# Performance work log

Hardware: AMD Instinct MI355X
Metric: run time of the kernel (lower is better)

Reference implementation:

```python
import jax, jax.numpy as jnp
import numpy as np

DIM = 1024
MLP_RATIO = 4
EPS = 1e-6


def rmsnorm(x, w):
    return x * jax.lax.rsqrt(jnp.mean(x * x, axis=-1, keepdims=True) + EPS) * w


def film(x, cond, w, b):
    # cond: [B, D] -> scale/shift: [B, D] each, broadcast over tokens
    ss = cond @ w + b  # [B, 2D]
    scale, shift = jnp.split(ss, 2, axis=-1)
    return x * (1.0 + scale[:, None, :]) + shift[:, None, :]


def setup_inputs() -> dict:
    key = jax.random.key(0)
    ks = jax.random.split(key, 16)
    B, N, D = 4, 2048, DIM
    H = D * MLP_RATIO
    s = lambda fan_in: 1.0 / np.sqrt(fan_in)
    return {
        "x": jax.random.normal(ks[0], (B, N, D), jnp.float32),
        "cond": jax.random.normal(ks[1], (B, D), jnp.float32),
        "norm1_w": jnp.ones((D,), jnp.float32),
        "film1_w": jax.random.normal(ks[2], (D, 2 * D), jnp.float32) * s(D),
        "film1_b": jnp.zeros((2 * D,), jnp.float32),
        "q_w": jax.random.normal(ks[3], (D, D), jnp.float32) * s(D),
        "q_b": jnp.zeros((D,), jnp.float32),
        "k_w": jax.random.normal(ks[4], (D, D), jnp.float32) * s(D),
        "k_b": jnp.zeros((D,), jnp.float32),
        "v_w": jax.random.normal(ks[5], (D, D), jnp.float32) * s(D),
        "v_b": jnp.zeros((D,), jnp.float32),
        "proj_w": jax.random.normal(ks[6], (D, D), jnp.float32) * s(D),
        "proj_b": jnp.zeros((D,), jnp.float32),
        "norm2_w": jnp.ones((D,), jnp.float32),
        "film2_w": jax.random.normal(ks[7], (D, 2 * D), jnp.float32) * s(D),
        "film2_b": jnp.zeros((2 * D,), jnp.float32),
        "mlp_w1": jax.random.normal(ks[8], (D, H), jnp.float32) * s(D),
        "mlp_b1": jnp.zeros((H,), jnp.float32),
        "mlp_w2": jax.random.normal(ks[9], (H, D), jnp.float32) * s(H),
        "mlp_b2": jnp.zeros((D,), jnp.float32),
    }


def reference(x, cond, norm1_w, film1_w, film1_b, q_w, q_b, k_w, k_b, v_w, v_b,
              proj_w, proj_b, norm2_w, film2_w, film2_b, mlp_w1, mlp_b1,
              mlp_w2, mlp_b2):
    B, N, D = x.shape
    x_in = x
    h = film(rmsnorm(x, norm1_w), cond, film1_w, film1_b)
    Q = h @ q_w + q_b
    K = h @ k_w + k_b
    V = h @ v_w + v_b
    scores = jnp.einsum('bnd,bmd->bnm', Q, K) * (D ** -0.5)  # [B,N,N]
    attn = jax.nn.softmax(scores, axis=-1)
    out = jnp.einsum('bnm,bmd->bnd', attn, V)
    x = x_in + (out @ proj_w + proj_b)
    x_in = x
    h = film(rmsnorm(x, norm2_w), cond, film2_w, film2_b)
    h = jax.nn.gelu(h @ mlp_w1 + mlp_b1, approximate=False) @ mlp_w2 + mlp_b2
    return x_in + h
```

## Files before the change

kernel.cpp:

```cpp
#include <hip/hip_runtime.h>
#include <math.h>

typedef unsigned short u16;
typedef __bf16 bf16;
typedef bf16 bf16x8 __attribute__((ext_vector_type(8)));
typedef float f32x4 __attribute__((ext_vector_type(4)));

#define DEV __device__ __forceinline__
#define MFMA(a, b, c) __builtin_amdgcn_mfma_f32_16x16x32_bf16(a, b, c, 0, 0, 0)

DEV u16 f2b(float f) {
  unsigned u = __builtin_bit_cast(unsigned, f);
  u += 0x7fffu + ((u >> 16) & 1u);
  return (u16)(u >> 16);
}
DEV float b2f(u16 h) {
  unsigned u = ((unsigned)h) << 16;
  return __builtin_bit_cast(float, u);
}
DEV float gelu_f(float x) {
  float e = __expf(x * (-1.5957691216f - 0.07135481283f * x * x));
  return x / (1.0f + e);
}

DEV void gl2lds16(const void* g, void* l) {
  __builtin_amdgcn_global_load_lds(
      (const __attribute__((address_space(1))) unsigned int*)g,
      (__attribute__((address_space(3))) unsigned int*)l, 16, 0, 0);
}

struct TDesc { const float* src; u16* dst; int R, C, t0, tx; };
struct T6 { TDesc d[6]; };

__global__ void k_transpose6(T6 td) {
  __shared__ float tile[32][33];
  const int id = blockIdx.x;
  TDesc d = td.d[0];
#pragma unroll
  for (int k = 1; k < 6; ++k)
    if (id >= td.d[k].t0) d = td.d[k];
  const int local = id - d.t0;
  const int c0 = (local % d.tx) * 32, r0 = (local / d.tx) * 32;
  const int tx = threadIdx.x, ty = threadIdx.y;
#pragma unroll
  for (int i = 0; i < 32; i += 8)
    tile[ty + i][tx] = d.src[(long)(r0 + ty + i) * d.C + c0 + tx];
  __syncthreads();
#pragma unroll
  for (int i = 0; i < 32; i += 8)
    d.dst[(long)(c0 + ty + i) * d.R + r0 + tx] = f2b(tile[tx][ty + i]);
}

__global__ __launch_bounds__(256) void k_film_part(const float* __restrict__ cond,
                                                   const float* __restrict__ f1w,
                                                   const float* __restrict__ f2w,
                                                   float* __restrict__ part) {
  const int j = blockIdx.x * 256 + threadIdx.x;
  const int b = blockIdx.y;
  const int z = blockIdx.z;
  const int kz = z & 7;
  const float* fw = (z < 8) ? f1w : f2w;
  const float* cp = cond + b * 1024 + kz * 128;
  const float* wp = fw + (long)kz * 128 * 2048 + j;
  float acc = 0.0f;
#pragma unroll 4
  for (int d = 0; d < 128; ++d) acc = fmaf(cp[d], wp[(long)d * 2048], acc);
  part[((z * 4 + b) << 11) + j] = acc;
}
__global__ __launch_bounds__(256) void k_film_comb(const float* __restrict__ part,
                                                   const float* __restrict__ f1b,
                                                   const float* __restrict__ f2b_,
                                                   float* __restrict__ ss) {
  const int j = blockIdx.x * 256 + threadIdx.x;
  const int b = blockIdx.y & 3, f = blockIdx.y >> 2;
  float a = (f ? f2b_ : f1b)[j];
#pragma unroll
  for (int kz = 0; kz < 8; ++kz) a += part[(((f * 8 + kz) * 4 + b) << 11) + j];
  ss[((f * 4 + b) << 11) + j] = a;
}

template <typename InT>
__global__ __launch_bounds__(256) void k_rmsfilm(const InT* __restrict__ x,
                                                 const float* __restrict__ nw,
                                                 const float* __restrict__ ss,
                                                 u16* __restrict__ h) {
  const int row = blockIdx.x;
  const int b = row >> 11;
  const int t = threadIdx.x;
  float4 v;
  if constexpr (sizeof(InT) == 4) {
    v = ((const float4*)(x + (long)row * 1024))[t];
  } else {
    ushort4 u = ((const ushort4*)(x + (long)row * 1024))[t];
    v = make_float4(b2f(u.x), b2f(u.y), b2f(u.z), b2f(u.w));
  }
  float s = v.x * v.x + v.y * v.y + v.z * v.z + v.w * v.w;
#pragma unroll
  for (int off = 32; off; off >>= 1) s += __shfl_xor(s, off);
  __shared__ float red[4];
  const int wv = t >> 6, lane = t & 63;
  if (lane == 0) red[wv] = s;
  __syncthreads();
  const float tot = red[0] + red[1] + red[2] + red[3];
  const float rn = rsqrtf(tot * (1.0f / 1024.0f) + 1e-6f);
  const float4 w4 = ((const float4*)nw)[t];
  const float4 sc = ((const float4*)(ss + b * 2048))[t];
  const float4 sh = ((const float4*)(ss + b * 2048 + 1024))[t];
  ushort4 o;
  o.x = f2b(v.x * rn * w4.x * (1.0f + sc.x) + sh.x);
  o.y = f2b(v.y * rn * w4.y * (1.0f + sc.y) + sh.y);
  o.z = f2b(v.z * rn * w4.z * (1.0f + sc.z) + sh.z);
  o.w = f2b(v.w * rn * w4.w * (1.0f + sc.w) + sh.w);
  ((ushort4*)(h + (long)row * 1024))[t] = o;
}

__global__ __launch_bounds__(256) void k_softmax(u16* __restrict__ S) {
  u16* p = S + ((long)blockIdx.x << 11);
  const int t = threadIdx.x;
  ushort4 u0 = ((ushort4*)p)[2 * t], u1 = ((ushort4*)p)[2 * t + 1];
  float f[8] = {b2f(u0.x), b2f(u0.y), b2f(u0.z), b2f(u0.w),
                b2f(u1.x), b2f(u1.y), b2f(u1.z), b2f(u1.w)};
  float m = f[0];
#pragma unroll
  for (int i = 1; i < 8; ++i) m = fmaxf(m, f[i]);
#pragma unroll
  for (int off = 32; off; off >>= 1) m = fmaxf(m, __shfl_xor(m, off));
  __shared__ float red[4];
  const int wv = t >> 6, lane = t & 63;
  if (lane == 0) red[wv] = m;
  __syncthreads();
  m = fmaxf(fmaxf(red[0], red[1]), fmaxf(red[2], red[3]));
  float s = 0.0f;
#pragma unroll
  for (int i = 0; i < 8; ++i) {
    f[i] = __expf(f[i] - m);
    s += f[i];
  }
#pragma unroll
  for (int off = 32; off; off >>= 1) s += __shfl_xor(s, off);
  __syncthreads();
  if (lane == 0) red[wv] = s;
  __syncthreads();
  const float inv = 1.0f / (red[0] + red[1] + red[2] + red[3]);
  ushort4 o0, o1;
  o0.x = f2b(f[0] * inv); o0.y = f2b(f[1] * inv);
  o0.z = f2b(f[2] * inv); o0.w = f2b(f[3] * inv);
  o1.x = f2b(f[4] * inv); o1.y = f2b(f[5] * inv);
  o1.z = f2b(f[6] * inv); o1.w = f2b(f[7] * inv);
  ((ushort4*)p)[2 * t] = o0;
  ((ushort4*)p)[2 * t + 1] = o1;
}

enum { EB = 1, ES = 2, EG = 4, ER = 8, EQKV = 16, ERB = 32 };

template <int EPI, typename OutT>
__global__ __launch_bounds__(256, 2) void k_gemm(
    const u16* __restrict__ A, const u16* __restrict__ B, OutT* __restrict__ C,
    const float* __restrict__ bias, const float* __restrict__ bias2,
    const float* __restrict__ bias3, const float* __restrict__ resid,
    u16* __restrict__ Vt, float scale, int N, int K, long sAb, long sBb, long sCb) {
  __shared__ u16 As[128 * 64];
  __shared__ u16 Bs[128 * 64];
  const int tid = threadIdx.x, lane = tid & 63, wv = tid >> 6;
  const int wr = wv >> 1, wc = wv & 1;
  const int r = lane & 15, q = lane >> 4;

  int flat = blockIdx.y * gridDim.x + blockIdx.x;
  const int nxy = gridDim.x * gridDim.y;
  flat = (flat & 7) * (nxy >> 3) + (flat >> 3);
  const int bx = flat % gridDim.x, by = flat / gridDim.x;

  const long bm = (long)by * 128, bn = (long)bx * 128;
  const u16* Ab = A + (long)blockIdx.z * sAb + bm * K;
  const u16* Bb = B + (long)blockIdx.z * sBb + bn * K;

  f32x4 acc[4][4] = {};

  for (int k0 = 0; k0 < K; k0 += 64) {
#pragma unroll
    for (int i = 0; i < 4; ++i) {
      const int c = i * 256 + tid;
      const int row = c >> 3, sp = c & 7;
      const long g = (long)row * K + k0 + ((sp ^ (row & 7)) << 3);
      gl2lds16(Ab + g, As + c * 8);
      gl2lds16(Bb + g, Bs + c * 8);
    }
    __syncthreads();
    bf16x8 a[8], b[8];
#pragma unroll
    for (int kh = 0; kh < 2; ++kh) {
#pragma unroll
      for (int i = 0; i < 4; ++i) {
        const int ar = wr * 64 + i * 16 + r;
        const int br = wc * 64 + i * 16 + r;
        a[kh * 4 + i] = *(const bf16x8*)&As[ar * 64 + ((kh * 4 + q) ^ (ar & 7)) * 8];
        b[kh * 4 + i] = *(const bf16x8*)&Bs[br * 64 + ((kh * 4 + q) ^ (br & 7)) * 8];
      }
    }
#pragma unroll
    for (int kh = 0; kh < 2; ++kh)
#pragma unroll
      for (int mi = 0; mi < 4; ++mi)
#pragma unroll
        for (int ni = 0; ni < 4; ++ni)
          acc[mi][ni] = MFMA(a[kh * 4 + mi], b[kh * 4 + ni], acc[mi][ni]);
    __syncthreads();
  }

  const long cb = (long)blockIdx.z * sCb;
#pragma unroll
  for (int ni = 0; ni < 4; ++ni) {
    const long col = bn + wc * 64 + ni * 16 + r;
    float bv = 0.0f;
    int reg = 0, c = (int)col;
    if constexpr ((EPI & EB) != 0) bv = bias[col];
    if constexpr ((EPI & EQKV) != 0) {
      reg = (int)(col >> 10);
      c = (int)col & 1023;
      bv = (reg == 0) ? bias[c] : (reg == 1) ? bias2[c] : bias3[c];
    }
#pragma unroll
    for (int mi = 0; mi < 4; ++mi) {
#pragma unroll
      for (int j = 0; j < 4; ++j) {
        const long row = bm + wr * 64 + mi * 16 + q * 4 + j;
        float v = acc[mi][ni][j];
        if constexpr ((EPI & ES) != 0) v *= scale;
        if constexpr ((EPI & (EB | EQKV)) != 0) v += bv;
        if constexpr ((EPI & EG) != 0) v = gelu_f(v);
        if constexpr ((EPI & ER) != 0) v += resid[row * N + col];
        if constexpr ((EPI & ERB) != 0) v += b2f(((const u16*)resid)[row * N + col]);
        if constexpr ((EPI & EQKV) != 0) {
          if (reg < 2)
            ((u16*)C)[(long)reg * 8388608 + row * 1024 + c] = f2b(v);
          else
            Vt[((row >> 11) << 21) + ((long)c << 11) + (row & 2047)] = f2b(v);
        } else if constexpr (sizeof(OutT) == 4) {
          C[cb + row * N + col] = v;
        } else {
          C[cb + row * N + col] = f2b(v);
        }
      }
    }
  }
}

extern "C" void kernel_launch(void* const* d_in, const int* in_sizes, int n_in,
                              void* d_out, int out_size, void* d_ws, size_t ws_size,
                              hipStream_t stream) {
  const float* x    = (const float*)d_in[0];
  const float* cond = (const float*)d_in[1];
  const float* n1w  = (const float*)d_in[2];
  const float* f1w  = (const float*)d_in[3];
  const float* f1b  = (const float*)d_in[4];
  const float* qw   = (const float*)d_in[5];
  const float* qb   = (const float*)d_in[6];
  const float* kw   = (const float*)d_in[7];
  const float* kb   = (const float*)d_in[8];
  const float* vw   = (const float*)d_in[9];
  const float* vb   = (const float*)d_in[10];
  const float* pw   = (const float*)d_in[11];
  const float* pb   = (const float*)d_in[12];
  const float* n2w  = (const float*)d_in[13];
  const float* f2w  = (const float*)d_in[14];
  const float* f2b_ = (const float*)d_in[15];
  const float* w1   = (const float*)d_in[16];
  const float* b1   = (const float*)d_in[17];
  const float* w2   = (const float*)d_in[18];
  const float* b2   = (const float*)d_in[19];
  float* out = (float*)d_out;

  char* ws = (char*)d_ws;
  size_t o = 0;
  auto alloc = [&](size_t bytes) {
    size_t ret = o;
    o += (bytes + 255) & ~(size_t)255;
    return ret;
  };
  const long N = 2048, D = 1024, H = 4096;

  u16* qkvT = (u16*)(ws + alloc(3 * D * D * 2));
  u16* pT   = (u16*)(ws + alloc(D * D * 2));
  u16* w1T  = (u16*)(ws + alloc(D * H * 2));
  u16* w2T  = (u16*)(ws + alloc(D * H * 2));
  float* ss   = (float*)(ws + alloc(2 * 4 * 2 * D * 4));
  float* part = (float*)(ws + alloc(16 * 4 * 2 * D * 4));
  u16* h    = (u16*)(ws + alloc(4 * N * D * 2));
  u16* x1b  = (u16*)(ws + alloc(4 * N * D * 2));
  u16* AO   = (u16*)(ws + alloc(4 * N * D * 2));
  const size_t big = o;
  u16* Q    = (u16*)(ws + alloc(4 * N * D * 2));
  u16* Kb   = (u16*)(ws + alloc(4 * N * D * 2));
  u16* Vt   = (u16*)(ws + alloc(4 * N * D * 2));
  u16* S    = (u16*)(ws + alloc(4 * N * N * 2));
  u16* h1   = (u16*)(ws + big);
  (void)ws_size; (void)in_sizes; (void)n_in; (void)out_size; (void)Kb;

  T6 td;
  td.d[0] = {qw, qkvT,                1024, 1024,    0,  32};
  td.d[1] = {kw, qkvT + 1024 * 1024,  1024, 1024, 1024,  32};
  td.d[2] = {vw, qkvT + 2048 * 1024,  1024, 1024, 2048,  32};
  td.d[3] = {pw, pT,                  1024, 1024, 3072,  32};
  td.d[4] = {w1, w1T,                 1024, 4096, 4096, 128};
  td.d[5] = {w2, w2T,                 4096, 1024, 8192,  32};
  k_transpose6<<<12288, dim3(32, 8), 0, stream>>>(td);

  k_film_part<<<dim3(8, 4, 16), 256, 0, stream>>>(cond, f1w, f2w, part);
  k_film_comb<<<dim3(8, 8), 256, 0, stream>>>(part, f1b, f2b_, ss);

  k_rmsfilm<float><<<8192, 256, 0, stream>>>(x, n1w, ss, h);

  k_gemm<EQKV, u16><<<dim3(24, 64, 1), 256, 0, stream>>>(
      h, qkvT, Q, qb, kb, vb, nullptr, Vt, 1.0f, 3072, 1024, 0, 0, 0);

  k_gemm<ES, u16><<<dim3(16, 16, 4), 256, 0, stream>>>(
      Q, Kb, S, nullptr, nullptr, nullptr, nullptr, nullptr, 0.03125f,
      2048, 1024, N * D, N * D, N * N);
  k_softmax<<<8192, 256, 0, stream>>>(S);

  k_gemm<0, u16><<<dim3(8, 16, 4), 256, 0, stream>>>(
      S, Vt, AO, nullptr, nullptr, nullptr, nullptr, nullptr, 1.0f,
      1024, 2048, N * N, D * N, N * D);

  k_gemm<EB | ER, u16><<<dim3(8, 64, 1), 256, 0, stream>>>(
      AO, pT, x1b, pb, nullptr, nullptr, x, nullptr, 1.0f, 1024, 1024, 0, 0, 0);

  k_rmsfilm<u16><<<8192, 256, 0, stream>>>(x1b, n2w, ss + 4 * 2048, h);

  k_gemm<EB | EG, u16><<<dim3(32, 64, 1), 256, 0, stream>>>(
      h, w1T, h1, b1, nullptr, nullptr, nullptr, nullptr, 1.0f, 4096, 1024, 0, 0, 0);

  k_gemm<EB | ERB, float><<<dim3(8, 64, 1), 256, 0, stream>>>(
      h1, w2T, out, b2, nullptr, nullptr, (const float*)x1b, nullptr, 1.0f, 1024, 4096, 0, 0, 0);
}
```

Measured before the change: 394.7 us.

## Split PV GEMM over K halves and fold the reduction into projection GEMM

The attention PV GEMM is split along its 2048-long key dimension into two 1024-wide halves. Each half writes its own partial output, which doubles the grid to 16x16x4 blocks. The projection GEMM then runs with K=2048 against a duplicated projection weight, so it sums the two partials itself. This targets low occupancy and a short grid in the PV GEMM. The cost is extra work and traffic in the projection GEMM, and the partials are rounded to bf16 before they are summed. Launch bounds also change from 2 to 4 blocks per CU, which may cause register pressure or spills.

Result: slower. 411.9 us (+4.4%).

```diff
diff --git a/kernel.cpp b/kernel.cpp
--- a/kernel.cpp
+++ b/kernel.cpp
@@ -29,7 +29,7 @@
       (__attribute__((address_space(3))) unsigned int*)l, 16, 0, 0);
 }
 
-struct TDesc { const float* src; u16* dst; int R, C, t0, tx; };
+struct TDesc { const float* src; u16* dst; int R, C, t0, tx, dstLd, dup; };
 struct T6 { TDesc d[6]; };
 
 __global__ void k_transpose6(T6 td) {
@@ -47,8 +47,12 @@
     tile[ty + i][tx] = d.src[(long)(r0 + ty + i) * d.C + c0 + tx];
   __syncthreads();
 #pragma unroll
-  for (int i = 0; i < 32; i += 8)
-    d.dst[(long)(c0 + ty + i) * d.R + r0 + tx] = f2b(tile[tx][ty + i]);
+  for (int i = 0; i < 32; i += 8) {
+    const u16 v = f2b(tile[tx][ty + i]);
+    u16* p = d.dst + (long)(c0 + ty + i) * d.dstLd + r0 + tx;
+    p[0] = v;
+    if (d.dup) p[d.R] = v;
+  }
 }
 
 __global__ __launch_bounds__(256) void k_film_part(const float* __restrict__ cond,
@@ -151,10 +155,10 @@
   ((ushort4*)p)[2 * t + 1] = o1;
 }
 
-enum { EB = 1, ES = 2, EG = 4, ER = 8, EQKV = 16, ERB = 32 };
+enum { EB = 1, ES = 2, EG = 4, ER = 8, EQKV = 16, ERB = 32, EPV = 64 };
 
 template <int EPI, typename OutT>
-__global__ __launch_bounds__(256, 2) void k_gemm(
+__global__ __launch_bounds__(256, 4) void k_gemm(
     const u16* __restrict__ A, const u16* __restrict__ B, OutT* __restrict__ C,
     const float* __restrict__ bias, const float* __restrict__ bias2,
     const float* __restrict__ bias3, const float* __restrict__ resid,
@@ -171,8 +175,11 @@
   const int bx = flat % gridDim.x, by = flat / gridDim.x;
 
   const long bm = (long)by * 128, bn = (long)bx * 128;
-  const u16* Ab = A + (long)blockIdx.z * sAb + bm * K;
-  const u16* Bb = B + (long)blockIdx.z * sBb + bn * K;
+  const long lda = (EPI & EPV) ? 2048 : K;
+  const long kof = (EPI & EPV) ? ((bn >> 10) << 10) : 0;
+  const long bnB = (EPI & EPV) ? (bn & 1023) : bn;
+  const u16* Ab = A + (long)blockIdx.z * sAb + bm * lda;
+  const u16* Bb = B + (long)blockIdx.z * sBb + bnB * lda;
 
   f32x4 acc[4][4] = {};
 
@@ -181,7 +188,7 @@
     for (int i = 0; i < 4; ++i) {
       const int c = i * 256 + tid;
       const int row = c >> 3, sp = c & 7;
-      const long g = (long)row * K + k0 + ((sp ^ (row & 7)) << 3);
+      const long g = (long)row * lda + kof + k0 + ((sp ^ (row & 7)) << 3);
       gl2lds16(Ab + g, As + c * 8);
       gl2lds16(Bb + g, Bs + c * 8);
     }
@@ -280,29 +287,29 @@
   const long N = 2048, D = 1024, H = 4096;
 
   u16* qkvT = (u16*)(ws + alloc(3 * D * D * 2));
-  u16* pT   = (u16*)(ws + alloc(D * D * 2));
+  u16* pT2  = (u16*)(ws + alloc(D * 2 * D * 2));
   u16* w1T  = (u16*)(ws + alloc(D * H * 2));
   u16* w2T  = (u16*)(ws + alloc(D * H * 2));
   float* ss   = (float*)(ws + alloc(2 * 4 * 2 * D * 4));
   float* part = (float*)(ws + alloc(16 * 4 * 2 * D * 4));
   u16* h    = (u16*)(ws + alloc(4 * N * D * 2));
   u16* x1b  = (u16*)(ws + alloc(4 * N * D * 2));
-  u16* AO   = (u16*)(ws + alloc(4 * N * D * 2));
   const size_t big = o;
   u16* Q    = (u16*)(ws + alloc(4 * N * D * 2));
   u16* Kb   = (u16*)(ws + alloc(4 * N * D * 2));
   u16* Vt   = (u16*)(ws + alloc(4 * N * D * 2));
   u16* S    = (u16*)(ws + alloc(4 * N * N * 2));
+  u16* AO2  = Q;
   u16* h1   = (u16*)(ws + big);
   (void)ws_size; (void)in_sizes; (void)n_in; (void)out_size; (void)Kb;
 
   T6 td;
-  td.d[0] = {qw, qkvT,                1024, 1024,    0,  32};
-  td.d[1] = {kw, qkvT + 1024 * 1024,  1024, 1024, 1024,  32};
-  td.d[2] = {vw, qkvT + 2048 * 1024,  1024, 1024, 2048,  32};
-  td.d[3] = {pw, pT,                  1024, 1024, 3072,  32};
-  td.d[4] = {w1, w1T,                 1024, 4096, 4096, 128};
-  td.d[5] = {w2, w2T,                 4096, 1024, 8192,  32};
+  td.d[0] = {qw, qkvT,                1024, 1024,    0,  32, 1024, 0};
+  td.d[1] = {kw, qkvT + 1024 * 1024,  1024, 1024, 1024,  32, 1024, 0};
+  td.d[2] = {vw, qkvT + 2048 * 1024,  1024, 1024, 2048,  32, 1024, 0};
+  td.d[3] = {pw, pT2,                 1024, 1024, 3072,  32, 2048, 1};
+  td.d[4] = {w1, w1T,                 1024, 4096, 4096, 128, 1024, 0};
+  td.d[5] = {w2, w2T,                 4096, 1024, 8192,  32, 4096, 0};
   k_transpose6<<<12288, dim3(32, 8), 0, stream>>>(td);
 
   k_film_part<<<dim3(8, 4, 16), 256, 0, stream>>>(cond, f1w, f2w, part);
@@ -318,12 +325,12 @@
       2048, 1024, N * D, N * D, N * N);
   k_softmax<<<8192, 256, 0, stream>>>(S);
 
-  k_gemm<0, u16><<<dim3(8, 16, 4), 256, 0, stream>>>(
-      S, Vt, AO, nullptr, nullptr, nullptr, nullptr, nullptr, 1.0f,
-      1024, 2048, N * N, D * N, N * D);
+  k_gemm<EPV, u16><<<dim3(16, 16, 4), 256, 0, stream>>>(
+      S, Vt, AO2, nullptr, nullptr, nullptr, nullptr, nullptr, 1.0f,
+      2048, 1024, N * N, D * N, N * 2048);
 
   k_gemm<EB | ER, u16><<<dim3(8, 64, 1), 256, 0, stream>>>(
-      AO, pT, x1b, pb, nullptr, nullptr, x, nullptr, 1.0f, 1024, 1024, 0, 0, 0);
+      AO2, pT2, x1b, pb, nullptr, nullptr, x, nullptr, 1.0f, 1024, 2048, 0, 0, 0);
 
   k_rmsfilm<u16><<<8192, 256, 0, stream>>>(x1b, n2w, ss + 4 * 2048, h);
 
```

## Fuse softmax exp into QK^T GEMM, defer normalization to PV epilogue

Applied to the files above, without the earlier changes.

Removes the standalone softmax pass. The QK^T GEMM epilogue now computes exp(score*scale) and writes per-tile row partial sums, a tiny kernel turns those into inverse row sums, and the PV GEMM multiplies by the inverse in its epilogue. There is no max subtraction, so exp can overflow for large scores; this relies on the scores being small for these inputs. The GEMM also gains a templated N tile (64 for the narrow-output GEMMs, giving more blocks) and a launch_bounds occupancy hint raised from 2 to 4.

Result: no change. 394.1 us (-0.2%).

```diff
diff --git a/kernel.cpp b/kernel.cpp
--- a/kernel.cpp
+++ b/kernel.cpp
@@ -114,53 +114,28 @@
   ((ushort4*)(h + (long)row * 1024))[t] = o;
 }
 
-__global__ __launch_bounds__(256) void k_softmax(u16* __restrict__ S) {
-  u16* p = S + ((long)blockIdx.x << 11);
-  const int t = threadIdx.x;
-  ushort4 u0 = ((ushort4*)p)[2 * t], u1 = ((ushort4*)p)[2 * t + 1];
-  float f[8] = {b2f(u0.x), b2f(u0.y), b2f(u0.z), b2f(u0.w),
-                b2f(u1.x), b2f(u1.y), b2f(u1.z), b2f(u1.w)};
-  float m = f[0];
-#pragma unroll
-  for (int i = 1; i < 8; ++i) m = fmaxf(m, f[i]);
-#pragma unroll
-  for (int off = 32; off; off >>= 1) m = fmaxf(m, __shfl_xor(m, off));
-  __shared__ float red[4];
-  const int wv = t >> 6, lane = t & 63;
-  if (lane == 0) red[wv] = m;
-  __syncthreads();
-  m = fmaxf(fmaxf(red[0], red[1]), fmaxf(red[2], red[3]));
+__global__ __launch_bounds__(256) void k_rowsuminv(const float* __restrict__ part,
+                                                   float* __restrict__ inv) {
+  const int id = blockIdx.x * 256 + threadIdx.x;
   float s = 0.0f;
 #pragma unroll
-  for (int i = 0; i < 8; ++i) {
-    f[i] = __expf(f[i] - m);
-    s += f[i];
-  }
-#pragma unroll
-  for (int off = 32; off; off >>= 1) s += __shfl_xor(s, off);
-  __syncthreads();
-  if (lane == 0) red[wv] = s;
-  __syncthreads();
-  const float inv = 1.0f / (red[0] + red[1] + red[2] + red[3]);
-  ushort4 o0, o1;
-  o0.x = f2b(f[0] * inv); o0.y = f2b(f[1] * inv);
-  o0.z = f2b(f[2] * inv); o0.w = f2b(f[3] * inv);
-  o1.x = f2b(f[4] * inv); o1.y = f2b(f[5] * inv);
-  o1.z = f2b(f[6] * inv); o1.w = f2b(f[7] * inv);
-  ((ushort4*)p)[2 * t] = o0;
-  ((ushort4*)p)[2 * t + 1] = o1;
-}
-
-enum { EB = 1, ES = 2, EG = 4, ER = 8, EQKV = 16, ERB = 32 };
-
-template <int EPI, typename OutT>
-__global__ __launch_bounds__(256, 2) void k_gemm(
+  for (int b = 0; b < 16; ++b) s += part[b * 8192 + id];
+  inv[id] = 1.0f / s;
+}
+
+enum { EB = 1, ES = 2, EG = 4, ER = 8, EQKV = 16, ERB = 32, EEXP = 64, EPVN = 128 };
+
+template <int BN, int EPI, typename OutT>
+__global__ __launch_bounds__(256, 4) void k_gemm(
     const u16* __restrict__ A, const u16* __restrict__ B, OutT* __restrict__ C,
     const float* __restrict__ bias, const float* __restrict__ bias2,
     const float* __restrict__ bias3, const float* __restrict__ resid,
-    u16* __restrict__ Vt, float scale, int N, int K, long sAb, long sBb, long sCb) {
+    u16* __restrict__ Vt, float* __restrict__ rsum, float scale,
+    int N, int K, long sAb, long sBb, long sCb) {
+  constexpr int NR = BN / 32;
+  constexpr int NBC = BN * 8 / 256;
   __shared__ u16 As[128 * 64];
-  __shared__ u16 Bs[128 * 64];
+  __shared__ u16 Bs[BN * 64];
   const int tid = threadIdx.x, lane = tid & 63, wv = tid >> 6;
   const int wr = wv >> 1, wc = wv & 1;
   const int r = lane & 15, q = lane >> 4;
@@ -170,11 +145,11 @@
   flat = (flat & 7) * (nxy >> 3) + (flat >> 3);
   const int bx = flat % gridDim.x, by = flat / gridDim.x;
 
-  const long bm = (long)by * 128, bn = (long)bx * 128;
+  const long bm = (long)by * 128, bn = (long)bx * BN;
   const u16* Ab = A + (long)blockIdx.z * sAb + bm * K;
   const u16* Bb = B + (long)blockIdx.z * sBb + bn * K;
 
-  f32x4 acc[4][4] = {};
+  f32x4 acc[4][NR] = {};
 
   for (int k0 = 0; k0 < K; k0 += 64) {
 #pragma unroll
@@ -183,34 +158,44 @@
       const int row = c >> 3, sp = c & 7;
       const long g = (long)row * K + k0 + ((sp ^ (row & 7)) << 3);
       gl2lds16(Ab + g, As + c * 8);
+    }
+#pragma unroll
+    for (int i = 0; i < NBC; ++i) {
+      const int c = i * 256 + tid;
+      const int row = c >> 3, sp = c & 7;
+      const long g = (long)row * K + k0 + ((sp ^ (row & 7)) << 3);
       gl2lds16(Bb + g, Bs + c * 8);
     }
     __syncthreads();
-    bf16x8 a[8], b[8];
+    bf16x8 a[8], b[2 * NR];
 #pragma unroll
     for (int kh = 0; kh < 2; ++kh) {
 #pragma unroll
       for (int i = 0; i < 4; ++i) {
         const int ar = wr * 64 + i * 16 + r;
-        const int br = wc * 64 + i * 16 + r;
         a[kh * 4 + i] = *(const bf16x8*)&As[ar * 64 + ((kh * 4 + q) ^ (ar & 7)) * 8];
-        b[kh * 4 + i] = *(const bf16x8*)&Bs[br * 64 + ((kh * 4 + q) ^ (br & 7)) * 8];
       }
+#pragma unroll
+      for (int ni = 0; ni < NR; ++ni) {
+        const int br = wc * (BN / 2) + ni * 16 + r;
+        b[kh * NR + ni] = *(const bf16x8*)&Bs[br * 64 + ((kh * 4 + q) ^ (br & 7)) * 8];
+      }
     }
 #pragma unroll
     for (int kh = 0; kh < 2; ++kh)
 #pragma unroll
       for (int mi = 0; mi < 4; ++mi)
 #pragma unroll
-        for (int ni = 0; ni < 4; ++ni)
-          acc[mi][ni] = MFMA(a[kh * 4 + mi], b[kh * 4 + ni], acc[mi][ni]);
+        for (int ni = 0; ni < NR; ++ni)
+          acc[mi][ni] = MFMA(a[kh * 4 + mi], b[kh * NR + ni], acc[mi][ni]);
     __syncthreads();
   }
 
   const long cb = (long)blockIdx.z * sCb;
-#pragma unroll
-  for (int ni = 0; ni < 4; ++ni) {
-    const long col = bn + wc * 64 + ni * 16 + r;
+  float rs[4][4] = {};
+#pragma unroll
+  for (int ni = 0; ni < NR; ++ni) {
+    const long col = bn + wc * (BN / 2) + ni * 16 + r;
     float bv = 0.0f;
     int reg = 0, c = (int)col;
     if constexpr ((EPI & EB) != 0) bv = bias[col];
@@ -226,6 +211,11 @@
         const long row = bm + wr * 64 + mi * 16 + q * 4 + j;
         float v = acc[mi][ni][j];
         if constexpr ((EPI & ES) != 0) v *= scale;
+        if constexpr ((EPI & EEXP) != 0) {
+          v = __expf(v * scale);
+          rs[mi][j] += v;
+        }
+        if constexpr ((EPI & EPVN) != 0) v *= bias[(long)blockIdx.z * 2048 + row];
         if constexpr ((EPI & (EB | EQKV)) != 0) v += bv;
         if constexpr ((EPI & EG) != 0) v = gelu_f(v);
         if constexpr ((EPI & ER) != 0) v += resid[row * N + col];
@@ -241,6 +231,32 @@
           C[cb + row * N + col] = f2b(v);
         }
       }
+    }
+  }
+  if constexpr ((EPI & EEXP) != 0) {
+    float* rbuf = (float*)As;
+#pragma unroll
+    for (int mi = 0; mi < 4; ++mi)
+#pragma unroll
+      for (int j = 0; j < 4; ++j) {
+        float v = rs[mi][j];
+        v += __shfl_xor(v, 1);
+        v += __shfl_xor(v, 2);
+        v += __shfl_xor(v, 4);
+        v += __shfl_xor(v, 8);
+        rs[mi][j] = v;
+      }
+    if (r == 0) {
+#pragma unroll
+      for (int mi = 0; mi < 4; ++mi)
+#pragma unroll
+        for (int j = 0; j < 4; ++j)
+          rbuf[wc * 128 + wr * 64 + mi * 16 + q * 4 + j] = rs[mi][j];
+    }
+    __syncthreads();
+    if (tid < 128) {
+      const float s = rbuf[tid] + rbuf[128 + tid];
+      rsum[(long)bx * 8192 + (long)blockIdx.z * 2048 + bm + tid] = s;
     }
   }
 }
@@ -283,8 +299,10 @@
   u16* pT   = (u16*)(ws + alloc(D * D * 2));
   u16* w1T  = (u16*)(ws + alloc(D * H * 2));
   u16* w2T  = (u16*)(ws + alloc(D * H * 2));
-  float* ss   = (float*)(ws + alloc(2 * 4 * 2 * D * 4));
-  float* part = (float*)(ws + alloc(16 * 4 * 2 * D * 4));
+  float* ss    = (float*)(ws + alloc(2 * 4 * 2 * D * 4));
+  float* part  = (float*)(ws + alloc(16 * 4 * 2 * D * 4));
+  float* spart = (float*)(ws + alloc(16 * 8192 * 4));
+  float* rsinv = (float*)(ws + alloc(8192 * 4));
   u16* h    = (u16*)(ws + alloc(4 * N * D * 2));
   u16* x1b  = (u16*)(ws + alloc(4 * N * D * 2));
   u16* AO   = (u16*)(ws + alloc(4 * N * D * 2));
@@ -310,26 +328,27 @@
 
   k_rmsfilm<float><<<8192, 256, 0, stream>>>(x, n1w, ss, h);
 
-  k_gemm<EQKV, u16><<<dim3(24, 64, 1), 256, 0, stream>>>(
-      h, qkvT, Q, qb, kb, vb, nullptr, Vt, 1.0f, 3072, 1024, 0, 0, 0);
-
-  k_gemm<ES, u16><<<dim3(16, 16, 4), 256, 0, stream>>>(
-      Q, Kb, S, nullptr, nullptr, nullptr, nullptr, nullptr, 0.03125f,
+  k_gemm<128, EQKV, u16><<<dim3(24, 64, 1), 256, 0, stream>>>(
+      h, qkvT, Q, qb, kb, vb, nullptr, Vt, nullptr, 1.0f, 3072, 1024, 0, 0, 0);
+
+  k_gemm<128, EEXP, u16><<<dim3(16, 16, 4), 256, 0, stream>>>(
+      Q, Kb, S, nullptr, nullptr, nullptr, nullptr, nullptr, spart, 0.03125f,
       2048, 1024, N * D, N * D, N * N);
-  k_softmax<<<8192, 256, 0, stream>>>(S);
-
-  k_gemm<0, u16><<<dim3(8, 16, 4), 256, 0, stream>>>(
-      S, Vt, AO, nullptr, nullptr, nullptr, nullptr, nullptr, 1.0f,
+  k_rowsuminv<<<32, 256, 0, stream>>>(spart, rsinv);
+
+  k_gemm<64, EPVN, u16><<<dim3(16, 16, 4), 256, 0, stream>>>(
+      S, Vt, AO, rsinv, nullptr, nullptr, nullptr, nullptr, nullptr, 1.0f,
       1024, 2048, N * N, D * N, N * D);
 
-  k_gemm<EB | ER, u16><<<dim3(8, 64, 1), 256, 0, stream>>>(
-      AO, pT, x1b, pb, nullptr, nullptr, x, nullptr, 1.0f, 1024, 1024, 0, 0, 0);
+  k_gemm<64, EB | ER, u16><<<dim3(16, 64, 1), 256, 0, stream>>>(
+      AO, pT, x1b, pb, nullptr, nullptr, x, nullptr, nullptr, 1.0f, 1024, 1024, 0, 0, 0);
 
   k_rmsfilm<u16><<<8192, 256, 0, stream>>>(x1b, n2w, ss + 4 * 2048, h);
 
-  k_gemm<EB | EG, u16><<<dim3(32, 64, 1), 256, 0, stream>>>(
-      h, w1T, h1, b1, nullptr, nullptr, nullptr, nullptr, 1.0f, 4096, 1024, 0, 0, 0);
-
-  k_gemm<EB | ERB, float><<<dim3(8, 64, 1), 256, 0, stream>>>(
-      h1, w2T, out, b2, nullptr, nullptr, (const float*)x1b, nullptr, 1.0f, 1024, 4096, 0, 0, 0);
-}
+  k_gemm<128, EB | EG, u16><<<dim3(32, 64, 1), 256, 0, stream>>>(
+      h, w1T, h1, b1, nullptr, nullptr, nullptr, nullptr, nullptr, 1.0f, 4096, 1024, 0, 0, 0);
+
+  k_gemm<64, EB | ERB, float><<<dim3(16, 64, 1), 256, 0, stream>>>(
+      h1, w2T, out, b2, nullptr, nullptr, (const float*)x1b, nullptr, nullptr, 1.0f,
+      1024, 4096, 0, 0, 0);
+}
```
